# Optimization experiments

Hardware: AMD Instinct MI355X
Metric: run time of the kernel (lower is better)

The kernel has to match this reference:

```python
import jax, jax.numpy as jnp
import numpy as np
from jax import lax


def _conv2d(x, w, b):
    # 3x3 conv, stride 1, pad 1, NCHW / OIHW
    out = lax.conv_general_dilated(x, w, (1, 1), ((1, 1), (1, 1)),
                                   dimension_numbers=('NCHW', 'OIHW', 'NCHW'))
    return out + b[None, :, None, None]


def _bilinear(img, py, px):
    # img: [C,H,W]; py,px: [K2,Ho,Wo] float sample coords -> [C,K2,Ho,Wo]
    H, W = img.shape[-2], img.shape[-1]
    y0 = jnp.floor(py); x0 = jnp.floor(px)
    wy1 = py - y0; wy0 = 1.0 - wy1
    wx1 = px - x0; wx0 = 1.0 - wx1

    def corner(yi, xi):
        valid = (yi >= 0) & (yi <= H - 1) & (xi >= 0) & (xi <= W - 1)
        yc = jnp.clip(yi, 0, H - 1).astype(jnp.int32)
        xc = jnp.clip(xi, 0, W - 1).astype(jnp.int32)
        return img[:, yc, xc] * valid.astype(img.dtype)  # [C,K2,Ho,Wo]

    return (wy0 * wx0 * corner(y0, x0) + wy0 * wx1 * corner(y0, x0 + 1)
            + wy1 * wx0 * corner(y0 + 1, x0) + wy1 * wx1 * corner(y0 + 1, x0 + 1))


def setup_inputs() -> dict:
    key = jax.random.key(0)
    ks = jax.random.split(key, 7)
    B, C, H, W = 8, 64, 128, 128
    O, K = 64, 3
    x = jax.random.normal(ks[0], (B, C, H, W), jnp.float32)
    # offset branch (torch init was zeros; use small random so offsets are nontrivial)
    w_off = jax.random.normal(ks[1], (2 * K * K, C, 3, 3), jnp.float32) * 0.01
    b_off = jax.random.normal(ks[2], (2 * K * K,), jnp.float32) * 0.01
    w_mask = jax.random.normal(ks[3], (K * K, C, 3, 3), jnp.float32) * 0.05
    b_mask = jnp.zeros((K * K,), jnp.float32)
    w_dcn = jax.random.normal(ks[4], (O, C, K, K), jnp.float32) * (1.0 / np.sqrt(C * K * K))
    b_dcn = jax.random.normal(ks[5], (O,), jnp.float32) * 0.01
    return {'x': x, 'w_off': w_off, 'b_off': b_off, 'w_mask': w_mask,
            'b_mask': b_mask, 'w_dcn': w_dcn, 'b_dcn': b_dcn}


def reference(x, w_off, b_off, w_mask, b_mask, w_dcn, b_dcn):
    B, C, H, W = x.shape
    K = 3; K2 = K * K; pad = 1; stride = 1
    offset = _conv2d(x, w_off, b_off)                 # [B,2*K2,H,W]
    mask = jax.nn.sigmoid(_conv2d(x, w_mask, b_mask))  # [B,K2,H,W]
    off = offset.reshape(B, K2, 2, H, W)
    dy, dx = off[:, :, 0], off[:, :, 1]               # [B,K2,H,W]
    ki = (jnp.arange(K2) // K).astype(x.dtype)
    kj = (jnp.arange(K2) % K).astype(x.dtype)
    base_y = jnp.arange(H, dtype=x.dtype)[None, :, None] * stride - pad + ki[:, None, None]  # [K2,H,1]
    base_x = jnp.arange(W, dtype=x.dtype)[None, None, :] * stride - pad + kj[:, None, None]  # [K2,1,W]
    py = base_y + dy                                   # [B,K2,H,W]
    px = base_x + dx
    sampled = jax.vmap(_bilinear)(x, py, px)           # [B,C,K2,H,W]
    sampled = sampled * mask[:, None]
    O = w_dcn.shape[0]
    out = jnp.einsum('bckhw,ock->bohw', sampled, w_dcn.reshape(O, C, K2))
    return out + b_dcn[None, :, None, None]
```

## Files before the change

### kernel.cpp

```cpp
#include <hip/hip_runtime.h>
#include <hip/hip_bf16.h>
#include <math.h>

#define Bt 8
#define Ct 64
#define Ht 128
#define Wt 128
#define Ot 64
#define HWt (Ht*Wt)

#define BROWS 20
#define BCOLS 12
#define BPX   240
#define WBASE_U 15360
#define ODM_B   30720

typedef __bf16 bf16x8 __attribute__((ext_vector_type(8)));
typedef float  f32x4  __attribute__((ext_vector_type(4)));

__device__ __forceinline__ uint f2bf_bits(float v) {
    uint u = __float_as_uint(v);
    uint lsb = (u >> 16) & 1u;
    return (u + 0x7fffu + lsb) >> 16;
}
__device__ __forceinline__ ushort f2bf(float v) {
    return (ushort)f2bf_bits(v);
}

__device__ __forceinline__ uint4 band_read(const ushort* smem, uint pIdx, uint chunkB) {
    uint off = pIdx * 128u + (chunkB ^ ((pIdx & 7u) << 4));
    return *(const uint4*)((const char*)smem + off);
}

__global__ __launch_bounds__(256) void prep_kernel(
    const float* __restrict__ x, const float* __restrict__ w_off,
    const float* __restrict__ w_mask, const float* __restrict__ w_dcn,
    ushort* __restrict__ xTb, ushort* __restrict__ wOffB, ushort* __restrict__ wMainB)
{
    int blk = blockIdx.x;
    int t = threadIdx.x;
    if (blk < 1024) {
        __shared__ float L[64][128];
        int b = blk & 7, y = blk >> 3;
        const float* xb = x + (size_t)b * 1048576 + y * 128;
#pragma unroll
        for (int it = 0; it < 8; ++it) {
            int i = it * 256 + t;
            int c = i >> 5, x4 = i & 31;
            *(float4*)&L[c][x4 * 4] = *(const float4*)&xb[(size_t)c * HWt + x4 * 4];
        }
        __syncthreads();
        int px = t >> 1, half = (t & 1) * 32;
        union { ushort u[32]; uint4 q[4]; } pk;
#pragma unroll
        for (int i = 0; i < 32; ++i) pk.u[i] = f2bf(L[half + i][px]);
        uint4* dst = (uint4*)(xTb + ((size_t)(b * 128 + y) * 128 + px) * 64 + half);
        dst[0] = pk.q[0]; dst[1] = pk.q[1]; dst[2] = pk.q[2]; dst[3] = pk.q[3];
    } else {
        int i = (blk - 1024) * 256 + t;
        if (i < 9 * 32 * 64) {
            int c = i & 63, ch = (i >> 6) & 31, k = i >> 11;
            float v = 0.f;
            if (ch < 18)      v = w_off[(ch * 64 + c) * 9 + k];
            else if (ch < 27) v = w_mask[((ch - 18) * 64 + c) * 9 + k];
            wOffB[i] = f2bf(v);
        } else {
            int j = i - 18432;
            if (j < 9 * 64 * 64) {
                int c = j & 63, o = (j >> 6) & 63, k = j >> 12;
                wMainB[j] = f2bf(w_dcn[(o * 64 + c) * 9 + k]);
            }
        }
    }
}

struct Tap { float w[4]; int pix[4]; uint gof[4]; uint inb; };

__device__ __forceinline__ void tap_ctx(int k, int ry, float cxf, int cq8,
                                        int row0, int col0,
                                        const float* __restrict__ odmRow, Tap& tp) {
    int ky = k / 3, kx = k - ky * 3;
    float dyv = odmRow[k];
    float dxv = odmRow[9 + k];
    float mkv = odmRow[18 + k];
    float py  = (float)(ry + ky - 1) + dyv;
    float pxf = cxf + (float)(kx - 1) + dxv;
    float y0f = floorf(py), x0f = floorf(pxf);
    float wy1 = py - y0f, wy0 = 1.f - wy1;
    float wx1 = pxf - x0f, wx0 = 1.f - wx1;
    bool vy0 = (y0f >= 0.f) && (y0f <= 127.f);
    bool vy1 = (y0f >= -1.f) && (y0f <= 126.f);
    bool vx0 = (x0f >= 0.f) && (x0f <= 127.f);
    bool vx1 = (x0f >= -1.f) && (x0f <= 126.f);
    tp.w[0] = (vy0 && vx0) ? wy0 * wx0 * mkv : 0.f;
    tp.w[1] = (vy0 && vx1) ? wy0 * wx1 * mkv : 0.f;
    tp.w[2] = (vy1 && vx0) ? wy1 * wx0 * mkv : 0.f;
    tp.w[3] = (vy1 && vx1) ? wy1 * wx1 * mkv : 0.f;
    int yi0 = (int)y0f, xi0 = (int)x0f;
    int y0c = min(max(yi0, 0), 127), y1c = min(max(yi0 + 1, 0), 127);
    int x0c = min(max(xi0, 0), 127), x1c = min(max(xi0 + 1, 0), 127);
    int by0 = y0c - row0, by1 = y1c - row0;
    int bx0 = x0c - col0, bx1 = x1c - col0;
    bool ry0 = (unsigned)by0 < (unsigned)BROWS, ry1 = (unsigned)by1 < (unsigned)BROWS;
    bool rx0 = (unsigned)bx0 < (unsigned)BCOLS, rx1 = (unsigned)bx1 < (unsigned)BCOLS;
    tp.inb = (uint)(ry0 && rx0) | ((uint)(ry0 && rx1) << 1)
           | ((uint)(ry1 && rx0) << 2) | ((uint)(ry1 && rx1) << 3);
    tp.pix[0] = by0 * BCOLS + bx0;
    tp.pix[1] = by0 * BCOLS + bx1;
    tp.pix[2] = by1 * BCOLS + bx0;
    tp.pix[3] = by1 * BCOLS + bx1;
    tp.gof[0] = (uint)(((y0c << 7) + x0c) * 64 + cq8);
    tp.gof[1] = (uint)(((y0c << 7) + x1c) * 64 + cq8);
    tp.gof[2] = (uint)(((y1c << 7) + x0c) * 64 + cq8);
    tp.gof[3] = (uint)(((y1c << 7) + x1c) * 64 + cq8);
}

__device__ __forceinline__ void tap_blend(const Tap& tp, const uint4* D, bf16x8* afr) {
    float w00 = tp.w[0], w01 = tp.w[1], w10 = tp.w[2], w11 = tp.w[3];
#pragma unroll
    for (int ks = 0; ks < 2; ++ks) {
        union { uint4 q; uint u[4]; } v00, v01, v10, v11, wr;
        v00.q = D[0 * 2 + ks];
        v01.q = D[1 * 2 + ks];
        v10.q = D[2 * 2 + ks];
        v11.q = D[3 * 2 + ks];
#pragma unroll
        for (int j = 0; j < 4; ++j) {
            float f00l = __uint_as_float(v00.u[j] << 16);
            float f00h = __uint_as_float(v00.u[j] & 0xffff0000u);
            float f01l = __uint_as_float(v01.u[j] << 16);
            float f01h = __uint_as_float(v01.u[j] & 0xffff0000u);
            float f10l = __uint_as_float(v10.u[j] << 16);
            float f10h = __uint_as_float(v10.u[j] & 0xffff0000u);
            float f11l = __uint_as_float(v11.u[j] << 16);
            float f11h = __uint_as_float(v11.u[j] & 0xffff0000u);
            float vl = w00 * f00l;
            vl = fmaf(w01, f01l, vl); vl = fmaf(w10, f10l, vl); vl = fmaf(w11, f11l, vl);
            float vh = w00 * f00h;
            vh = fmaf(w01, f01h, vh); vh = fmaf(w10, f10h, vh); vh = fmaf(w11, f11h, vh);
            wr.u[j] = (f2bf_bits(vh) << 16) | f2bf_bits(vl);
        }
        afr[ks] = __builtin_bit_cast(bf16x8, wr.q);
    }
}

__global__ __launch_bounds__(512, 4) void dcn_fused_kernel(
    const ushort* __restrict__ xTb, const ushort* __restrict__ wOffB,
    const ushort* __restrict__ wMainB, const float* __restrict__ b_off,
    const float* __restrict__ b_mask, const float* __restrict__ b_dcn,
    float* __restrict__ out)
{
    __shared__ ushort smem[33792];
    float* odmF = (float*)((char*)smem + ODM_B);

    int t = threadIdx.x;
    int blk = blockIdx.x;
    int b = blk & 7;
    int tile = blk >> 3;
    int rowBase = (tile >> 4) * 16;
    int colBase = (tile & 15) * 8;
    int wv = t >> 6, ln = t & 63;
    int m = ln & 15, cq = ln >> 4;
    int cq8 = cq * 8;
    int prow = 2 * wv + (m >> 3);
    int pcol = m & 7;
    int ry = rowBase + prow;
    int cx = colBase + pcol;

    const ushort* xbb = xTb + (size_t)b * 1048576;

#pragma unroll
    for (int it = 0; it < 4; ++it) {
        int j = it * 512 + t;
        if (j < BPX * 8) {
            int pIdx = j >> 3, ch8 = j & 7;
            int br = pIdx / BCOLS, bc = pIdx - br * BCOLS;
            int iy = min(max(rowBase - 2 + br, 0), 127);
            int ix = min(max(colBase - 2 + bc, 0), 127);
            *(uint4*)((char*)smem + pIdx * 128 + ((ch8 * 16) ^ ((pIdx & 7) << 4))) =
                *(const uint4*)&xbb[(size_t)((iy << 7) + ix) * 64 + ch8 * 8];
        }
    }
#pragma unroll
    for (int it = 0; it < 5; ++it) {
        int j = it * 512 + t;
        if (j < 2304) {
            int row = j >> 3, gch = j & 7;
            int col = ((gch + row) & 7) * 8;
            *(uint4*)&smem[WBASE_U + row * 64 + col] = *(const uint4*)&wOffB[(size_t)row * 64 + gch * 8];
        }
    }
    __syncthreads();

    {
        f32x4 acc0 = {0.f, 0.f, 0.f, 0.f};
        f32x4 acc1 = {0.f, 0.f, 0.f, 0.f};
#pragma unroll
        for (int k = 0; k < 9; ++k) {
            int ky = k / 3, kx = k - ky * 3;
            int iyr = prow + ky - 1;
            int ixr = pcol + kx - 1;
            bool ok = ((unsigned)(rowBase + iyr) < 128u) && ((unsigned)(colBase + ixr) < 128u);
            uint pIdx = (uint)((iyr + 2) * BCOLS + (ixr + 2));
            uint4 a0 = band_read(smem, pIdx, cq8 * 2);
            uint4 a1 = band_read(smem, pIdx, cq8 * 2 + 64);
            if (!ok) { a0 = uint4{0u,0u,0u,0u}; a1 = uint4{0u,0u,0u,0u}; }
            int br0 = k * 32 + m;
            int br1 = br0 + 16;
#pragma unroll
            for (int ks = 0; ks < 2; ++ks) {
                bf16x8 afr = __builtin_bit_cast(bf16x8, ks ? a1 : a0);
                int gs = ks * 4 + cq;
                bf16x8 b0 = __builtin_bit_cast(bf16x8,
                    *(const uint4*)&smem[WBASE_U + br0 * 64 + ((gs + br0) & 7) * 8]);
                bf16x8 b1 = __builtin_bit_cast(bf16x8,
                    *(const uint4*)&smem[WBASE_U + br1 * 64 + ((gs + br1) & 7) * 8]);
                acc0 = __builtin_amdgcn_mfma_f32_16x16x32_bf16(afr, b0, acc0, 0, 0, 0);
                acc1 = __builtin_amdgcn_mfma_f32_16x16x32_bf16(afr, b1, acc1, 0, 0, 0);
            }
        }
        __syncthreads();

        int n = m;
        int pxl = wv * 16 + (cq << 2);
#pragma unroll
        for (int r = 0; r < 4; ++r) {
            int pp = pxl + r;
            odmF[pp * 28 + (n & 1) * 9 + (n >> 1)] = acc0[r] + b_off[n];
            int ch = 16 + n;
            float v1 = acc1[r];
            if (ch < 18) {
                odmF[pp * 28 + (ch & 1) * 9 + (ch >> 1)] = v1 + b_off[ch];
            } else if (ch < 27) {
                float val = v1 + b_mask[ch - 18];
                odmF[pp * 28 + 18 + (ch - 18)] = 1.f / (1.f + __expf(-val));
            }
        }
        __syncthreads();
    }

    f32x4 acc[4];
#pragma unroll
    for (int i = 0; i < 4; ++i) acc[i] = f32x4{0.f, 0.f, 0.f, 0.f};

    float cxf = (float)cx;
    const float* odmRow = odmF + (wv * 16 + m) * 28;
    const int row0 = rowBase - 2, col0 = colBase - 2;
    const ushort* wmk = wMainB + (size_t)m * 64 + cq8;

#pragma unroll
    for (int k = 0; k < 9; ++k) {
        Tap tp;
        tap_ctx(k, ry, cxf, cq8, row0, col0, odmRow, tp);

        uint4 D[8];
#pragma unroll
        for (int c = 0; c < 4; ++c) {
            bool ib = (tp.inb >> c) & 1u;
            uint pS = ib ? (uint)tp.pix[c] : 0u;
            D[c * 2]     = band_read(smem, pS, cq8 * 2);
            D[c * 2 + 1] = band_read(smem, pS, cq8 * 2 + 64);
            if (!ib) {
                D[c * 2]     = *(const uint4*)(xbb + tp.gof[c]);
                D[c * 2 + 1] = *(const uint4*)(xbb + tp.gof[c] + 32);
            }
        }

        bf16x8 afr[2];
        tap_blend(tp, D, afr);

        const ushort* wk = wmk + (size_t)k * 4096;
#pragma unroll
        for (int ks = 0; ks < 2; ++ks) {
#pragma unroll
            for (int nt = 0; nt < 4; ++nt) {
                bf16x8 bb = __builtin_bit_cast(bf16x8,
                    *(const uint4*)(wk + nt * 1024 + ks * 32));
                acc[nt] = __builtin_amdgcn_mfma_f32_16x16x32_bf16(afr[ks], bb, acc[nt], 0, 0, 0);
            }
        }
    }

#pragma unroll
    for (int nt = 0; nt < 4; ++nt) {
        int o = nt * 16 + m;
        float bias = b_dcn[o];
        float4 v;
        v.x = acc[nt][0] + bias;
        v.y = acc[nt][1] + bias;
        v.z = acc[nt][2] + bias;
        v.w = acc[nt][3] + bias;
        float* orow = out + ((size_t)(b * 64 + o) << 14)
                    + (rowBase + 2 * wv + (cq >> 1)) * 128 + colBase + (cq & 1) * 4;
        *(float4*)orow = v;
    }
}

extern "C" void kernel_launch(void* const* d_in, const int* in_sizes, int n_in,
                              void* d_out, int out_size, void* d_ws, size_t ws_size,
                              hipStream_t stream) {
    const float* x      = (const float*)d_in[0];
    const float* w_off  = (const float*)d_in[1];
    const float* b_off  = (const float*)d_in[2];
    const float* w_mask = (const float*)d_in[3];
    const float* b_mask = (const float*)d_in[4];
    const float* w_dcn  = (const float*)d_in[5];
    const float* b_dcn  = (const float*)d_in[6];
    float* out = (float*)d_out;

    ushort* xTb    = (ushort*)d_ws;
    ushort* wOffB  = xTb + (size_t)Bt * HWt * 64;
    ushort* wMainB = wOffB + 18432;

    hipLaunchKernelGGL(prep_kernel, dim3(1024 + 216), dim3(256), 0, stream,
                       x, w_off, w_mask, w_dcn, xTb, wOffB, wMainB);
    hipLaunchKernelGGL(dcn_fused_kernel, dim3(1024), dim3(512), 0, stream,
                       xTb, wOffB, wMainB, b_off, b_mask, b_dcn, out);
}
```

Baseline: 174.8 us.

## Stream weights through a small shared buffer per tap to raise occupancy

Shrinks LDS from ~67KB to ~52KB by staging offset-conv weights two taps at a time, and main DCN weights one tap at a time, in a single reused 8KB buffer. Launch bounds go from 4 to 6 blocks per CU, and the odm stride goes from 28 to 27. Main-conv weights now come from LDS instead of global memory. The cost is many extra __syncthreads and global-to-LDS copies per tap, which serialise load and compute.

```diff
diff --git a/kernel.cpp b/kernel.cpp
--- a/kernel.cpp
+++ b/kernel.cpp
@@ -12,8 +12,9 @@
 #define BROWS 20
 #define BCOLS 12
 #define BPX   240
-#define WBASE_U 15360
-#define ODM_B   30720
+#define WBUF_U 15360
+#define ODM_B  38912
+#define ODM_S  27
 
 typedef __bf16 bf16x8 __attribute__((ext_vector_type(8)));
 typedef float  f32x4  __attribute__((ext_vector_type(4)));
@@ -144,13 +145,13 @@
     }
 }
 
-__global__ __launch_bounds__(512, 4) void dcn_fused_kernel(
+__global__ __launch_bounds__(512, 6) void dcn_fused_kernel(
     const ushort* __restrict__ xTb, const ushort* __restrict__ wOffB,
     const ushort* __restrict__ wMainB, const float* __restrict__ b_off,
     const float* __restrict__ b_mask, const float* __restrict__ b_dcn,
     float* __restrict__ out)
 {
-    __shared__ ushort smem[33792];
+    __shared__ ushort smem[26368];
     float* odmF = (float*)((char*)smem + ODM_B);
 
     int t = threadIdx.x;
@@ -181,75 +182,100 @@
                 *(const uint4*)&xbb[(size_t)((iy << 7) + ix) * 64 + ch8 * 8];
         }
     }
-#pragma unroll
-    for (int it = 0; it < 5; ++it) {
-        int j = it * 512 + t;
-        if (j < 2304) {
-            int row = j >> 3, gch = j & 7;
-            int col = ((gch + row) & 7) * 8;
-            *(uint4*)&smem[WBASE_U + row * 64 + col] = *(const uint4*)&wOffB[(size_t)row * 64 + gch * 8];
-        }
+    {
+        int r = t >> 3, gch = t & 7;
+        *(uint4*)&smem[WBUF_U + r * 64 + ((gch + r) & 7) * 8] =
+            *(const uint4*)&wOffB[(size_t)r * 64 + gch * 8];
     }
     __syncthreads();
 
+    f32x4 acc0 = {0.f, 0.f, 0.f, 0.f};
+    f32x4 acc1 = {0.f, 0.f, 0.f, 0.f};
+#pragma unroll
+    for (int kp = 0; kp < 5; ++kp) {
+        if (kp > 0) {
+            __syncthreads();
+            const int nchunks = (kp == 4) ? 256 : 512;
+            if (t < nchunks) {
+                int r = t >> 3, gch = t & 7;
+                *(uint4*)&smem[WBUF_U + r * 64 + ((gch + r) & 7) * 8] =
+                    *(const uint4*)&wOffB[(size_t)(kp * 64 + r) * 64 + gch * 8];
+            }
+            __syncthreads();
+        }
+#pragma unroll
+        for (int tl = 0; tl < 2; ++tl) {
+            const int k = kp * 2 + tl;
+            if (k <= 8) {
+                int ky = k / 3, kx = k - ky * 3;
+                int iyr = prow + ky - 1;
+                int ixr = pcol + kx - 1;
+                bool ok = ((unsigned)(rowBase + iyr) < 128u) && ((unsigned)(colBase + ixr) < 128u);
+                uint pIdx = (uint)((iyr + 2) * BCOLS + (ixr + 2));
+                uint4 a0 = band_read(smem, pIdx, cq8 * 2);
+                uint4 a1 = band_read(smem, pIdx, cq8 * 2 + 64);
+                if (!ok) { a0 = uint4{0u,0u,0u,0u}; a1 = uint4{0u,0u,0u,0u}; }
+                int lbr0 = tl * 32 + m;
+                int lbr1 = lbr0 + 16;
+#pragma unroll
+                for (int ks = 0; ks < 2; ++ks) {
+                    bf16x8 afr = __builtin_bit_cast(bf16x8, ks ? a1 : a0);
+                    int gs = ks * 4 + cq;
+                    bf16x8 b0 = __builtin_bit_cast(bf16x8,
+                        *(const uint4*)&smem[WBUF_U + lbr0 * 64 + ((gs + lbr0) & 7) * 8]);
+                    bf16x8 b1 = __builtin_bit_cast(bf16x8,
+                        *(const uint4*)&smem[WBUF_U + lbr1 * 64 + ((gs + lbr1) & 7) * 8]);
+                    acc0 = __builtin_amdgcn_mfma_f32_16x16x32_bf16(afr, b0, acc0, 0, 0, 0);
+                    acc1 = __builtin_amdgcn_mfma_f32_16x16x32_bf16(afr, b1, acc1, 0, 0, 0);
+                }
+            }
+        }
+    }
+
     {
-        f32x4 acc0 = {0.f, 0.f, 0.f, 0.f};
-        f32x4 acc1 = {0.f, 0.f, 0.f, 0.f};
-#pragma unroll
-        for (int k = 0; k < 9; ++k) {
-            int ky = k / 3, kx = k - ky * 3;
-            int iyr = prow + ky - 1;
-            int ixr = pcol + kx - 1;
-            bool ok = ((unsigned)(rowBase + iyr) < 128u) && ((unsigned)(colBase + ixr) < 128u);
-            uint pIdx = (uint)((iyr + 2) * BCOLS + (ixr + 2));
-            uint4 a0 = band_read(smem, pIdx, cq8 * 2);
-            uint4 a1 = band_read(smem, pIdx, cq8 * 2 + 64);
-            if (!ok) { a0 = uint4{0u,0u,0u,0u}; a1 = uint4{0u,0u,0u,0u}; }
-            int br0 = k * 32 + m;
-            int br1 = br0 + 16;
-#pragma unroll
-            for (int ks = 0; ks < 2; ++ks) {
-                bf16x8 afr = __builtin_bit_cast(bf16x8, ks ? a1 : a0);
-                int gs = ks * 4 + cq;
-                bf16x8 b0 = __builtin_bit_cast(bf16x8,
-                    *(const uint4*)&smem[WBASE_U + br0 * 64 + ((gs + br0) & 7) * 8]);
-                bf16x8 b1 = __builtin_bit_cast(bf16x8,
-                    *(const uint4*)&smem[WBASE_U + br1 * 64 + ((gs + br1) & 7) * 8]);
-                acc0 = __builtin_amdgcn_mfma_f32_16x16x32_bf16(afr, b0, acc0, 0, 0, 0);
-                acc1 = __builtin_amdgcn_mfma_f32_16x16x32_bf16(afr, b1, acc1, 0, 0, 0);
-            }
-        }
-        __syncthreads();
-
         int n = m;
         int pxl = wv * 16 + (cq << 2);
 #pragma unroll
         for (int r = 0; r < 4; ++r) {
             int pp = pxl + r;
-            odmF[pp * 28 + (n & 1) * 9 + (n >> 1)] = acc0[r] + b_off[n];
+            odmF[pp * ODM_S + (n & 1) * 9 + (n >> 1)] = acc0[r] + b_off[n];
             int ch = 16 + n;
             float v1 = acc1[r];
             if (ch < 18) {
-                odmF[pp * 28 + (ch & 1) * 9 + (ch >> 1)] = v1 + b_off[ch];
+                odmF[pp * ODM_S + (ch & 1) * 9 + (ch >> 1)] = v1 + b_off[ch];
             } else if (ch < 27) {
                 float val = v1 + b_mask[ch - 18];
-                odmF[pp * 28 + 18 + (ch - 18)] = 1.f / (1.f + __expf(-val));
-            }
-        }
-        __syncthreads();
-    }
+                odmF[pp * ODM_S + 18 + (ch - 18)] = 1.f / (1.f + __expf(-val));
+            }
+        }
+    }
+    __syncthreads();
+
+    {
+        int r = t >> 3, gch = t & 7;
+        *(uint4*)&smem[WBUF_U + r * 64 + ((gch + r) & 7) * 8] =
+            *(const uint4*)&wMainB[(size_t)r * 64 + gch * 8];
+    }
+    __syncthreads();
 
     f32x4 acc[4];
 #pragma unroll
     for (int i = 0; i < 4; ++i) acc[i] = f32x4{0.f, 0.f, 0.f, 0.f};
 
     float cxf = (float)cx;
-    const float* odmRow = odmF + (wv * 16 + m) * 28;
+    const float* odmRow = odmF + (wv * 16 + m) * ODM_S;
     const int row0 = rowBase - 2, col0 = colBase - 2;
-    const ushort* wmk = wMainB + (size_t)m * 64 + cq8;
 
 #pragma unroll
     for (int k = 0; k < 9; ++k) {
+        if (k > 0) {
+            __syncthreads();
+            int r = t >> 3, gch = t & 7;
+            *(uint4*)&smem[WBUF_U + r * 64 + ((gch + r) & 7) * 8] =
+                *(const uint4*)&wMainB[(size_t)(k * 64 + r) * 64 + gch * 8];
+            __syncthreads();
+        }
+
         Tap tp;
         tap_ctx(k, ry, cxf, cq8, row0, col0, odmRow, tp);
 
@@ -269,13 +295,14 @@
         bf16x8 afr[2];
         tap_blend(tp, D, afr);
 
-        const ushort* wk = wmk + (size_t)k * 4096;
 #pragma unroll
         for (int ks = 0; ks < 2; ++ks) {
+            int chk = ks * 4 + cq;
 #pragma unroll
             for (int nt = 0; nt < 4; ++nt) {
+                int lrow = nt * 16 + m;
                 bf16x8 bb = __builtin_bit_cast(bf16x8,
-                    *(const uint4*)(wk + nt * 1024 + ks * 32));
+                    *(const uint4*)&smem[WBUF_U + lrow * 64 + ((chk + lrow) & 7) * 8]);
                 acc[nt] = __builtin_amdgcn_mfma_f32_16x16x32_bf16(afr[ks], bb, acc[nt], 0, 0, 0);
             }
         }
```

New measurement: 146.4 us. 16.3% less time.
